# Kernel tuning notes

Measured on AMD Instinct MI355X. Metric: run time of the kernel, lower is better.

The kernel has to match this reference:

```python
import jax, jax.numpy as jnp
import numpy as np

THRESH = 0.5
RADIUS = 4  # maxpool kernel = 2*RADIUS+1 = 9


def setup_inputs() -> dict:
    key = jax.random.key(0)
    H = W = 8192
    pred_vol = jax.random.uniform(key, (H, W), dtype=jnp.float32)
    return {"pred_vol": pred_vol}


def reference(pred_vol):
    # Faithful translation of Postprocess.forward up through conf_vol
    # (the threshold + 9x9 local-max pooling + equality-compare peak map).
    # The original's torch.nonzero / numpy coordinate extraction is a
    # data-dependent-shape host-side epilogue and is not part of the
    # dense kernel; the dense conf_vol fully determines it.
    k = 2 * RADIUS + 1
    # threshold: keep values strictly above thresh, else 0
    pred_thresh = jnp.where(pred_vol > THRESH, pred_vol, 0.0)
    # local max pool, stride 1, SAME-style padding with -inf (matches
    # torch MaxPool2d implicit -inf padding)
    mp = jax.lax.reduce_window(
        pred_thresh,
        -jnp.inf,
        jax.lax.max,
        window_dimensions=(k, k),
        window_strides=(1, 1),
        padding=((RADIUS, RADIUS), (RADIUS, RADIUS)),
    )
    # keep only positions that are both positive and the local maximum
    conf_vol = jnp.where((mp > 0.0) & (mp == pred_thresh), mp, 0.0)
    return conf_vol
```

## Files before the change

### kernel.cpp

```cpp
#include <hip/hip_runtime.h>


#define W 8192
#define H 8192
#define THRESH 0.5f
#define SR 32

typedef float v4f __attribute__((ext_vector_type(4)));

__device__ __forceinline__ v4f ld4(const float* __restrict__ in, int r, int c) {
    v4f v = {0.f, 0.f, 0.f, 0.f};
    if ((unsigned)c < (unsigned)W) {
        v = *(const v4f*)(in + (size_t)r * W + c);
    }
    return v;
}

__global__ __launch_bounds__(256, 4) void peak_stream(const float* __restrict__ in,
                                                      float* __restrict__ out) {
    const int lane = threadIdx.x;
    const int col0 = blockIdx.x * 256 + lane * 4;
    const int r0   = (blockIdx.y * 4 + threadIdx.y) * SR;

    v4f hm[9];
    int fl[9];

    auto dorow = [&](int rin, int k, bool emit) {
        v4f l = {0.f, 0.f, 0.f, 0.f}, v = l, r = l;
        if ((unsigned)rin < (unsigned)H) {
            l = ld4(in, rin, col0 - 4);
            v = ld4(in, rin, col0);
            r = ld4(in, rin, col0 + 4);
        }
        const float common = fmaxf(fmaxf(fmaxf(l.w, v.x), fmaxf(v.y, v.z)),
                                   fmaxf(v.w, r.x));
        const float m12  = fmaxf(l.y, l.z);
        const float m910 = fmaxf(r.y, r.z);
        v4f o;
        o.x = fmaxf(common, fmaxf(l.x, m12));
        o.y = fmaxf(common, fmaxf(m12, r.y));
        o.z = fmaxf(common, fmaxf(l.z, m910));
        o.w = fmaxf(common, fmaxf(m910, r.w));
        hm[k] = o;
        fl[k] = (o.x == v.x ? 1 : 0) | (o.y == v.y ? 2 : 0) |
                (o.z == v.z ? 4 : 0) | (o.w == v.w ? 8 : 0);
        if (emit) {
            v4f m = hm[0];
#pragma unroll
            for (int j = 1; j < 9; ++j) {
                m.x = fmaxf(m.x, hm[j].x);
                m.y = fmaxf(m.y, hm[j].y);
                m.z = fmaxf(m.z, hm[j].z);
                m.w = fmaxf(m.w, hm[j].w);
            }
            const v4f hc = hm[(k + 5) % 9];
            const int fc = fl[(k + 5) % 9];
            v4f ov;
            ov.x = (m.x > THRESH && m.x == hc.x && (fc & 1)) ? m.x : 0.f;
            ov.y = (m.y > THRESH && m.y == hc.y && (fc & 2)) ? m.y : 0.f;
            ov.z = (m.z > THRESH && m.z == hc.z && (fc & 4)) ? m.z : 0.f;
            ov.w = (m.w > THRESH && m.w == hc.w && (fc & 8)) ? m.w : 0.f;
            const int rout = rin - 4;
            __builtin_nontemporal_store(ov, (v4f*)(out + (size_t)rout * W + col0));
        }
    };

#pragma unroll
    for (int t = 0; t < 9; ++t) {
        dorow(r0 - 4 + t, t, t >= 8);
    }
#pragma unroll
    for (int tc = 9; tc + 9 <= SR + 8; tc += 9) {
#pragma unroll
        for (int k = 0; k < 9; ++k) {
            dorow(r0 - 4 + tc + k, k, true);
        }
    }
#pragma unroll
    for (int k = 0; k < SR + 8 - 36; ++k) {
        dorow(r0 - 4 + 36 + k, k, true);
    }
}

extern "C" void kernel_launch(void* const* d_in, const int* in_sizes, int n_in,
                              void* d_out, int out_size, void* d_ws, size_t ws_size,
                              hipStream_t stream) {
    const float* in = (const float*)d_in[0];
    float* out = (float*)d_out;
    dim3 grid(W / 256, H / (4 * SR));
    dim3 block(64, 4, 1);
    peak_stream<<<grid, block, 0, stream>>>(in, out);
}
```

Baseline: 451.0 us.

## Stream input rows through per-wave LDS ring via async global_load_lds prefetch

Replaces the three overlapping direct global vector loads per row with asynchronous global-to-LDS loads into a per-wave nine-slot ring buffer. Rows are prefetched nine ahead and gated with manual vmcnt waits. The wave's strip height also doubles to cut halo re-reads. This aims to hide memory latency and remove redundant halo loads, at the cost of hand-tuned waitcnt values that are fragile and extra LDS usage that may limit occupancy.

```diff
diff --git a/kernel.cpp b/kernel.cpp
--- a/kernel.cpp
+++ b/kernel.cpp
@@ -4,34 +4,62 @@
 #define W 8192
 #define H 8192
 #define THRESH 0.5f
-#define SR 32
+#define SR 64
+#define SLOTS 9
+#define RB 268
+#define WAVES 4
 
 typedef float v4f __attribute__((ext_vector_type(4)));
 
-__device__ __forceinline__ v4f ld4(const float* __restrict__ in, int r, int c) {
-    v4f v = {0.f, 0.f, 0.f, 0.f};
-    if ((unsigned)c < (unsigned)W) {
-        v = *(const v4f*)(in + (size_t)r * W + c);
-    }
-    return v;
+template <int N>
+__device__ __forceinline__ void wait_vm() {
+    asm volatile("s_waitcnt vmcnt(%0)" :: "n"(N) : "memory");
+}
+__device__ __forceinline__ void wait_lgkm0() {
+    asm volatile("s_waitcnt lgkmcnt(0)" ::: "memory");
 }
 
 __global__ __launch_bounds__(256, 4) void peak_stream(const float* __restrict__ in,
                                                       float* __restrict__ out) {
-    const int lane = threadIdx.x;
-    const int col0 = blockIdx.x * 256 + lane * 4;
-    const int r0   = (blockIdx.y * 4 + threadIdx.y) * SR;
+    __shared__ float smem[WAVES * SLOTS * RB];
+    const int lane  = threadIdx.x;
+    const int bcol0 = blockIdx.x * 256;
+    const int col0  = bcol0 + lane * 4;
+    const int r0    = (blockIdx.y * WAVES + threadIdx.y) * SR;
+    const int rlast = r0 + SR + 3;
+    float* const ring = smem + threadIdx.y * (SLOTS * RB);
 
-    v4f hm[9];
-    int fl[9];
+    const int c1 = bcol0 - 4 + lane * 4;
+    const bool m1 = (c1 >= 0);
+    const int c2 = bcol0 + 252 + lane * 4;
+    const bool a2 = (lane < 3) && (c2 + 4 <= W);
+    const bool z2 = (lane < 3) && (c2 + 4 > W);
 
-    auto dorow = [&](int rin, int k, bool emit) {
-        v4f l = {0.f, 0.f, 0.f, 0.f}, v = l, r = l;
+    auto prefetch = [&](int rp, int slot) {
+        int rpc = rp < rlast ? rp : rlast;
+        rpc = rpc < 0 ? 0 : (rpc >= H ? H - 1 : rpc);
+        const float* row = in + (size_t)rpc * W;
+        float* const dst = ring + slot * RB;
+        if (m1) __builtin_amdgcn_global_load_lds(row + c1, dst, 16, 0, 0);
+        if (a2) __builtin_amdgcn_global_load_lds(row + c2, dst + 256, 16, 0, 0);
+        if (!m1) *(v4f*)(dst + 4 * lane) = (v4f){0.f, 0.f, 0.f, 0.f};
+        if (z2)  *(v4f*)(dst + 256 + 4 * lane) = (v4f){0.f, 0.f, 0.f, 0.f};
+    };
+
+    v4f hm[SLOTS];
+    int fl[SLOTS];
+
+    auto consume = [&](int rin, int k, bool emit) {
+        v4f l, v, r;
         if ((unsigned)rin < (unsigned)H) {
-            l = ld4(in, rin, col0 - 4);
-            v = ld4(in, rin, col0);
-            r = ld4(in, rin, col0 + 4);
+            const float* rowp = ring + k * RB + 4 * lane;
+            l = *(const v4f*)(rowp);
+            v = *(const v4f*)(rowp + 4);
+            r = *(const v4f*)(rowp + 8);
+        } else {
+            l = v = r = (v4f){0.f, 0.f, 0.f, 0.f};
         }
+        wait_lgkm0();
         const float common = fmaxf(fmaxf(fmaxf(l.w, v.x), fmaxf(v.y, v.z)),
                                    fmaxf(v.w, r.x));
         const float m12  = fmaxf(l.y, l.z);
@@ -66,19 +94,21 @@
     };
 
 #pragma unroll
-    for (int t = 0; t < 9; ++t) {
-        dorow(r0 - 4 + t, t, t >= 8);
-    }
-#pragma unroll
-    for (int tc = 9; tc + 9 <= SR + 8; tc += 9) {
+    for (int t = 0; t < 9; ++t) prefetch(r0 - 4 + t, t);
+
+#define C0(K) wait_vm<16>();     consume(r0 - 4 + K, K, K >= 8); prefetch(r0 + 5 + K, K);
+#define C1(K) wait_vm<17 + K>(); consume(r0 + 5 + K, K, true);   prefetch(r0 + 14 + K, K);
+    C0(0) C0(1) C0(2) C0(3) C0(4) C0(5) C0(6) C0(7) C0(8)
+    C1(0) C1(1) C1(2) C1(3) C1(4) C1(5) C1(6) C1(7) C1(8)
+#undef C0
+#undef C1
+    for (int tc = 18; tc < 72; tc += 9) {
 #pragma unroll
         for (int k = 0; k < 9; ++k) {
-            dorow(r0 - 4 + tc + k, k, true);
+            wait_vm<25>();
+            consume(r0 - 4 + tc + k, k, true);
+            prefetch(r0 + 5 + tc + k, k);
         }
-    }
-#pragma unroll
-    for (int k = 0; k < SR + 8 - 36; ++k) {
-        dorow(r0 - 4 + 36 + k, k, true);
     }
 }
 
@@ -87,7 +117,7 @@
                               hipStream_t stream) {
     const float* in = (const float*)d_in[0];
     float* out = (float*)d_out;
-    dim3 grid(W / 256, H / (4 * SR));
-    dim3 block(64, 4, 1);
+    dim3 grid(W / 256, H / (WAVES * SR));
+    dim3 block(64, WAVES, 1);
     peak_stream<<<grid, block, 0, stream>>>(in, out);
 }
```

New measurement: 453.8 us. No clear change (+0.6%).
